# Kernel tuning notes

Hardware: AMD Instinct MI355X
Metric: run time of the kernel (lower is better)

The kernel has to match this reference:

```python
import jax, jax.numpy as jnp
import numpy as np

ALPHA = 0.2          # LeakyReLU negative slope
NEG_BIG = -9e15      # mask value from original code


def setup_inputs() -> dict:
    key = jax.random.key(0)
    k1, k2, k3, k4 = jax.random.split(key, 4)
    B, N, F_in, F_out = 16, 1024, 256, 256
    x = jax.random.normal(k1, (B, N, F_in), dtype=jnp.float32)
    adj = jax.random.randint(k2, (B, N, N), 0, 2, dtype=jnp.int32)
    # xavier-uniform-like scales
    W = jax.random.normal(k3, (F_in, F_out), dtype=jnp.float32) * np.sqrt(2.0 / (F_in + F_out))
    a = jax.random.normal(k4, (2 * F_out, 1), dtype=jnp.float32) * np.sqrt(2.0 / (2 * F_out + 1))
    return {"x": x, "adj": adj, "W": W, "a": a}


def reference(x, adj, W, a):
    # x: [B,N,Fin], adj: [B,N,N] (int mask), W: [Fin,Fout], a: [2*Fout,1]
    F_out = a.shape[0] // 2
    h = jnp.einsum("bni,io->bno", x, W)            # [B,N,Fout]
    # Decompose a into left/right halves: e_ij = lrelu(a_l.h_i + a_r.h_j)
    a_l = a[:F_out, 0]                               # [Fout]
    a_r = a[F_out:, 0]                               # [Fout]
    el = h @ a_l                                     # [B,N] score contribution of target i
    er = h @ a_r                                     # [B,N] score contribution of source j
    e = jax.nn.leaky_relu(el[:, :, None] + er[:, None, :], ALPHA)  # [B,N,N]
    e = jnp.where(adj > 0, e, NEG_BIG)
    attn = jax.nn.softmax(e, axis=-1)                # masked softmax over neighbors j
    # weighted sum of neighbor features; concat with n_heads=1 is identity
    return jnp.einsum("bij,bjo->bio", attn, h)       # [B,N,Fout]
```

## Files before the change

kernel.cpp:

```cpp
#include <hip/hip_runtime.h>
#include <stdint.h>

#define ALPHA 0.2f

typedef __attribute__((ext_vector_type(8))) short bf16x8;
typedef __attribute__((ext_vector_type(8))) unsigned short u16x8;
typedef __attribute__((ext_vector_type(4))) float f32x4;

__device__ __forceinline__ unsigned short f2bf(float f) {
    unsigned int u = __float_as_uint(f);
    u += 0x7fffu + ((u >> 16) & 1u);
    return (unsigned short)(u >> 16);
}

__device__ __forceinline__ void gload_lds16(const void* g, void* l) {
    __builtin_amdgcn_global_load_lds(
        (const __attribute__((address_space(1))) unsigned int*)g,
        (__attribute__((address_space(3))) unsigned int*)l, 16, 0, 0);
}

__global__ void wt_wa_kernel(const float* __restrict__ W,
                             const float* __restrict__ a,
                             unsigned short* __restrict__ Wtbf,
                             float* __restrict__ wa) {
    const int t = threadIdx.x;
    if (blockIdx.x < 256) {
        const int o = blockIdx.x;
        Wtbf[o * 256 + t] = f2bf(W[t * 256 + o]);
    } else {
        float sl = 0.f, sr = 0.f;
        const float* wr = W + t * 256;
        for (int o = 0; o < 256; ++o) {
            const float wv = wr[o];
            sl += wv * a[o];
            sr += wv * a[256 + o];
        }
        wa[t] = sl;
        wa[256 + t] = sr;
    }
}

__global__ __launch_bounds__(256) void gemm_hx(
    const unsigned short* __restrict__ Wtbf,
    const float* __restrict__ x,
    const float* __restrict__ wa,
    unsigned short* __restrict__ hT,
    float* __restrict__ el, float* __restrict__ er)
{
    __shared__ __align__(16) unsigned short As[64 * 256];
    __shared__ float wa_s[512];

    const int tid = threadIdx.x;
    const int w = tid >> 6, l = tid & 63;
    const int q = l >> 4, ml = l & 15;
    const int wm = (w >> 1) * 32;
    const int wn = (w & 1) * 64;
    const int m0 = blockIdx.y * 64;
    const int n0 = blockIdx.x * 128;

    if (tid < 128) *(float4*)(wa_s + tid * 4) = *(const float4*)(wa + tid * 4);

    for (int rd = 0; rd < 8; ++rd) {
        const int cb = rd * 256 + (w << 6);
        const int p = cb + l;
        const int r = p >> 5;
        const int c = p & 31;
        gload_lds16(Wtbf + (size_t)(m0 + r) * 256 + ((c ^ (r & 7)) << 3),
                    As + cb * 8);
    }
    __syncthreads();

    const bool do_e = (blockIdx.y == 0) && (w < 2);

    f32x4 acc[2][4];
    for (int i = 0; i < 2; ++i)
        for (int j = 0; j < 4; ++j) {
            f32x4 z = {0.f, 0.f, 0.f, 0.f};
            acc[i][j] = z;
        }
    float sl[4] = {0.f, 0.f, 0.f, 0.f};
    float sr[4] = {0.f, 0.f, 0.f, 0.f};

    for (int k0 = 0; k0 < 256; k0 += 64) {
        bf16x8 aF[2][2], bF[2][4];
#pragma unroll
        for (int ks = 0; ks < 2; ++ks) {
            const int kb = k0 + ks * 32 + q * 8;
#pragma unroll
            for (int mt = 0; mt < 2; ++mt) {
                const int row = wm + mt * 16 + ml;
                const int cf = (kb >> 3) ^ (row & 7);
                aF[ks][mt] = *(const bf16x8*)(As + (row * 32 + cf) * 8);
            }
#pragma unroll
            for (int nt = 0; nt < 4; ++nt) {
                const int grow = n0 + wn + nt * 16 + ml;
                const float* xp = x + (size_t)grow * 256 + kb;
                const float4 v0 = *(const float4*)(xp);
                const float4 v1 = *(const float4*)(xp + 4);
                bf16x8 f;
                f[0] = (short)f2bf(v0.x); f[1] = (short)f2bf(v0.y);
                f[2] = (short)f2bf(v0.z); f[3] = (short)f2bf(v0.w);
                f[4] = (short)f2bf(v1.x); f[5] = (short)f2bf(v1.y);
                f[6] = (short)f2bf(v1.z); f[7] = (short)f2bf(v1.w);
                bF[ks][nt] = f;
                if (do_e) {
                    const float* wl = wa_s + kb;
                    const float* wrr = wa_s + 256 + kb;
                    sl[nt] += v0.x * wl[0] + v0.y * wl[1] + v0.z * wl[2] + v0.w * wl[3]
                            + v1.x * wl[4] + v1.y * wl[5] + v1.z * wl[6] + v1.w * wl[7];
                    sr[nt] += v0.x * wrr[0] + v0.y * wrr[1] + v0.z * wrr[2] + v0.w * wrr[3]
                            + v1.x * wrr[4] + v1.y * wrr[5] + v1.z * wrr[6] + v1.w * wrr[7];
                }
            }
        }
#pragma unroll
        for (int ks = 0; ks < 2; ++ks)
            for (int mt = 0; mt < 2; ++mt)
                for (int nt = 0; nt < 4; ++nt)
                    acc[mt][nt] = __builtin_amdgcn_mfma_f32_16x16x32_bf16(
                        aF[ks][mt], bF[ks][nt], acc[mt][nt], 0, 0, 0);
    }

    if (do_e) {
#pragma unroll
        for (int nt = 0; nt < 4; ++nt) {
            sl[nt] += __shfl_xor(sl[nt], 16); sl[nt] += __shfl_xor(sl[nt], 32);
            sr[nt] += __shfl_xor(sr[nt], 16); sr[nt] += __shfl_xor(sr[nt], 32);
        }
        if (l < 16) {
#pragma unroll
            for (int nt = 0; nt < 4; ++nt) {
                const int n = n0 + wn + nt * 16 + l;
                el[n] = sl[nt];
                er[n] = sr[nt];
            }
        }
    }

    for (int mt = 0; mt < 2; ++mt)
        for (int nt = 0; nt < 4; ++nt) {
            const int gn = n0 + wn + nt * 16 + ml;
            for (int r = 0; r < 4; ++r) {
                const int gm = m0 + wm + mt * 16 + q * 4 + r;
                hT[(size_t)gm * 16384 + gn] = f2bf(acc[mt][nt][r]);
            }
        }
}

__global__ __launch_bounds__(256) void pv_fused(
    const int* __restrict__ adj,
    const float* __restrict__ el,
    const float* __restrict__ er,
    const unsigned short* __restrict__ hT,
    float* __restrict__ out)
{
    __shared__ float er_s[1024];
    __shared__ float el_s[32];
    __shared__ float c_s[32];
    __shared__ __align__(16) unsigned short pk_s[32 * 64];
    __shared__ __align__(16) unsigned char buf[8192];
    __shared__ __align__(16) unsigned short Hs[256 * 64];

    unsigned char (*nibs)[256] = (unsigned char (*)[256])buf;
    unsigned short* Ps = (unsigned short*)buf;

    const int tid = threadIdx.x;
    const int w = tid >> 6, l = tid & 63;
    const int q = l >> 4, ml = l & 15;
    const int b = blockIdx.y;
    const int i0 = blockIdx.x * 32;

    *(float4*)(er_s + tid * 4) = *(const float4*)(er + (b << 10) + tid * 4);
    if (tid < 32) el_s[tid] = el[(b << 10) + i0 + tid];
    __syncthreads();

    const float NINF = -__builtin_inff();
    const float* erb = er + (b << 10);
    for (int rr = 0; rr < 8; ++rr) {
        const int row = w * 8 + rr;
        const int* arow = adj + (size_t)((b << 10) + i0 + row) * 1024;
        const float eli = el_s[row];

        int4 av[4]; float4 erv[4];
#pragma unroll
        for (int it = 0; it < 4; ++it) {
            const int j = it * 256 + l * 4;
            av[it]  = *(const int4*)(arow + j);
            erv[it] = *(const float4*)(erb + j);
        }
        float s = 0.f;
#pragma unroll
        for (int it = 0; it < 4; ++it) {
            float e0 = eli + erv[it].x; e0 = e0 > 0.f ? e0 : ALPHA * e0;
            float e1 = eli + erv[it].y; e1 = e1 > 0.f ? e1 : ALPHA * e1;
            float e2 = eli + erv[it].z; e2 = e2 > 0.f ? e2 : ALPHA * e2;
            float e3 = eli + erv[it].w; e3 = e3 > 0.f ? e3 : ALPHA * e3;
            e0 = av[it].x > 0 ? e0 : NINF;
            e1 = av[it].y > 0 ? e1 : NINF;
            e2 = av[it].z > 0 ? e2 : NINF;
            e3 = av[it].w > 0 ? e3 : NINF;
            s += __expf(e0) + __expf(e1) + __expf(e2) + __expf(e3);
            nibs[row][it * 64 + l] =
                (unsigned char)((av[it].x > 0) | ((av[it].y > 0) << 1) |
                                ((av[it].z > 0) << 2) | ((av[it].w > 0) << 3));
        }
#pragma unroll
        for (int off = 32; off >= 1; off >>= 1) s += __shfl_xor(s, off);
        if (l == 0) c_s[row] = __logf(s);
    }
    for (int rr = 0; rr < 8; ++rr) {
        const int row = w * 8 + rr;
        const unsigned nr = *(const unsigned int*)(&nibs[row][l * 4]);
        pk_s[row * 64 + l] =
            (unsigned short)((nr & 0xFu) | ((nr >> 4) & 0xF0u) |
                             ((nr >> 8) & 0xF00u) | ((nr >> 12) & 0xF000u));
    }
    __syncthreads();

    const int ib = tid >> 3;
    const int js = (tid & 7) * 8;
    const float eli_b = el_s[ib];
    const float ci = c_s[ib];

    f32x4 acc[2][4];
    for (int i = 0; i < 2; ++i)
        for (int j = 0; j < 4; ++j) {
            f32x4 z = {0.f, 0.f, 0.f, 0.f};
            acc[i][j] = z;
        }

    const unsigned short* hb = hT + (size_t)b * 1024;

    for (int j0 = 0; j0 < 1024; j0 += 64) {
        for (int cr = 0; cr < 8; ++cr) {
            const int cb = cr * 256 + (w << 6);
            const int p = cb + l;
            const int r = p >> 3;
            const int cc = (p & 7) ^ (r & 7);
            gload_lds16(hb + (size_t)r * 16384 + j0 + cc * 8, Hs + cb * 8);
        }
        {
            const unsigned hw = pk_s[ib * 64 + ((j0 + js) >> 4)];
            const unsigned v = (hw >> ((j0 + js) & 15)) & 0xFFu;
            u16x8 pvv;
#pragma unroll
            for (int u = 0; u < 8; ++u) {
                float e = eli_b + er_s[j0 + js + u];
                e = e > 0.f ? e : ALPHA * e;
                const float p = ((v >> u) & 1u) ? __expf(e - ci) : 0.f;
                pvv[u] = f2bf(p);
            }
            *(u16x8*)(Ps + ib * 72 + js) = pvv;
        }
        __syncthreads();

        bf16x8 aF[2][2], bF[2][4];
#pragma unroll
        for (int ks = 0; ks < 2; ++ks) {
#pragma unroll
            for (int mt = 0; mt < 2; ++mt)
                aF[ks][mt] = *(const bf16x8*)(Ps + (mt * 16 + ml) * 72 + ks * 32 + q * 8);
#pragma unroll
            for (int nt = 0; nt < 4; ++nt) {
                const int oc = (w << 6) + nt * 16 + ml;
                bF[ks][nt] = *(const bf16x8*)(Hs + (oc * 8 + ((ks * 4 + q) ^ (oc & 7))) * 8);
            }
        }
#pragma unroll
        for (int ks = 0; ks < 2; ++ks)
            for (int mt = 0; mt < 2; ++mt)
                for (int nt = 0; nt < 4; ++nt)
                    acc[mt][nt] = __builtin_amdgcn_mfma_f32_16x16x32_bf16(
                        aF[ks][mt], bF[ks][nt], acc[mt][nt], 0, 0, 0);
        __syncthreads();
    }

    float* ob = out + (size_t)b * 262144;
    for (int mt = 0; mt < 2; ++mt)
        for (int nt = 0; nt < 4; ++nt) {
            const int gn = (w << 6) + nt * 16 + ml;
            for (int r = 0; r < 4; ++r) {
                const int gm = i0 + mt * 16 + q * 4 + r;
                ob[(size_t)gm * 256 + gn] = acc[mt][nt][r];
            }
        }
}

extern "C" void kernel_launch(void* const* d_in, const int* in_sizes, int n_in,
                              void* d_out, int out_size, void* d_ws, size_t ws_size,
                              hipStream_t stream) {
    const float* x   = (const float*)d_in[0];
    const int*   adj = (const int*)d_in[1];
    const float* W   = (const float*)d_in[2];
    const float* a   = (const float*)d_in[3];
    float* out = (float*)d_out;

    char* ws = (char*)d_ws;
    unsigned short* Wtbf = (unsigned short*)(ws);
    float* wa            = (float*)(ws + 131072);
    unsigned short* h_T  = (unsigned short*)(ws + 133120);
    float* el            = (float*)(ws + 8521728);
    float* er            = (float*)(ws + 8587264);

    wt_wa_kernel<<<dim3(257), dim3(256), 0, stream>>>(W, a, Wtbf, wa);

    gemm_hx<<<dim3(128, 4), dim3(256), 0, stream>>>(Wtbf, x, wa, h_T, el, er);

    pv_fused<<<dim3(32, 16), dim3(256), 0, stream>>>(adj, el, er, h_T, out);
}
```

Baseline: 163.2 us.

## Split adjacency mask/softmax-normalizer pass into a separate high-parallelism kernel

Moves the adjacency read, bit-packing and log-sum-exp normalizer computation out of the fused PV kernel into a standalone mask_kernel with one wave per row across 4096 blocks. The PV kernel then loads a small precomputed 16-bit packed mask and per-row constants instead of streaming the 64MB int adjacency itself. The aim is to spread the bandwidth-bound adjacency scan over many more blocks than the 512-block PV grid. The cost is an extra kernel launch and a workspace round trip for the packed mask and normalizers.

```diff
diff --git a/kernel.cpp b/kernel.cpp
--- a/kernel.cpp
+++ b/kernel.cpp
@@ -148,22 +148,70 @@
         }
 }
 
-__global__ __launch_bounds__(256) void pv_fused(
+__global__ __launch_bounds__(256) void mask_kernel(
     const int* __restrict__ adj,
     const float* __restrict__ el,
     const float* __restrict__ er,
+    float* __restrict__ c,
+    unsigned short* __restrict__ pk16)
+{
+    __shared__ unsigned char nibs[4][256];
+
+    const int w = threadIdx.x >> 6, l = threadIdx.x & 63;
+    const int row = blockIdx.x * 4 + w;
+    const int b = row >> 10;
+    const int* arow = adj + (size_t)row * 1024;
+    const float* erb = er + (b << 10);
+    const float eli = el[row];
+
+    int4 av[4]; float4 erv[4];
+#pragma unroll
+    for (int it = 0; it < 4; ++it) {
+        const int j = it * 256 + l * 4;
+        av[it]  = *(const int4*)(arow + j);
+        erv[it] = *(const float4*)(erb + j);
+    }
+
+    const float NINF = -__builtin_inff();
+    float s = 0.f;
+#pragma unroll
+    for (int it = 0; it < 4; ++it) {
+        float e0 = eli + erv[it].x; e0 = e0 > 0.f ? e0 : ALPHA * e0;
+        float e1 = eli + erv[it].y; e1 = e1 > 0.f ? e1 : ALPHA * e1;
+        float e2 = eli + erv[it].z; e2 = e2 > 0.f ? e2 : ALPHA * e2;
+        float e3 = eli + erv[it].w; e3 = e3 > 0.f ? e3 : ALPHA * e3;
+        e0 = av[it].x > 0 ? e0 : NINF;
+        e1 = av[it].y > 0 ? e1 : NINF;
+        e2 = av[it].z > 0 ? e2 : NINF;
+        e3 = av[it].w > 0 ? e3 : NINF;
+        s += __expf(e0) + __expf(e1) + __expf(e2) + __expf(e3);
+        nibs[w][it * 64 + l] =
+            (unsigned char)((av[it].x > 0) | ((av[it].y > 0) << 1) |
+                            ((av[it].z > 0) << 2) | ((av[it].w > 0) << 3));
+    }
+#pragma unroll
+    for (int off = 32; off >= 1; off >>= 1) s += __shfl_xor(s, off);
+    if (l == 0) c[row] = __logf(s);
+
+    const unsigned nr = *(const unsigned int*)(&nibs[w][l * 4]);
+    const unsigned short mask16 =
+        (unsigned short)((nr & 0xFu) | ((nr >> 4) & 0xF0u) |
+                         ((nr >> 8) & 0xF00u) | ((nr >> 12) & 0xF000u));
+    pk16[(size_t)row * 64 + l] = mask16;
+}
+
+__global__ __launch_bounds__(256) void pv_kernel(
+    const unsigned short* __restrict__ pk16,
+    const float* __restrict__ el,
+    const float* __restrict__ er,
+    const float* __restrict__ c,
     const unsigned short* __restrict__ hT,
     float* __restrict__ out)
 {
     __shared__ float er_s[1024];
-    __shared__ float el_s[32];
-    __shared__ float c_s[32];
     __shared__ __align__(16) unsigned short pk_s[32 * 64];
-    __shared__ __align__(16) unsigned char buf[8192];
     __shared__ __align__(16) unsigned short Hs[256 * 64];
-
-    unsigned char (*nibs)[256] = (unsigned char (*)[256])buf;
-    unsigned short* Ps = (unsigned short*)buf;
+    __shared__ __align__(16) unsigned short Ps[32 * 72];
 
     const int tid = threadIdx.x;
     const int w = tid >> 6, l = tid & 63;
@@ -172,56 +220,13 @@
     const int i0 = blockIdx.x * 32;
 
     *(float4*)(er_s + tid * 4) = *(const float4*)(er + (b << 10) + tid * 4);
-    if (tid < 32) el_s[tid] = el[(b << 10) + i0 + tid];
-    __syncthreads();
-
-    const float NINF = -__builtin_inff();
-    const float* erb = er + (b << 10);
-    for (int rr = 0; rr < 8; ++rr) {
-        const int row = w * 8 + rr;
-        const int* arow = adj + (size_t)((b << 10) + i0 + row) * 1024;
-        const float eli = el_s[row];
-
-        int4 av[4]; float4 erv[4];
-#pragma unroll
-        for (int it = 0; it < 4; ++it) {
-            const int j = it * 256 + l * 4;
-            av[it]  = *(const int4*)(arow + j);
-            erv[it] = *(const float4*)(erb + j);
-        }
-        float s = 0.f;
-#pragma unroll
-        for (int it = 0; it < 4; ++it) {
-            float e0 = eli + erv[it].x; e0 = e0 > 0.f ? e0 : ALPHA * e0;
-            float e1 = eli + erv[it].y; e1 = e1 > 0.f ? e1 : ALPHA * e1;
-            float e2 = eli + erv[it].z; e2 = e2 > 0.f ? e2 : ALPHA * e2;
-            float e3 = eli + erv[it].w; e3 = e3 > 0.f ? e3 : ALPHA * e3;
-            e0 = av[it].x > 0 ? e0 : NINF;
-            e1 = av[it].y > 0 ? e1 : NINF;
-            e2 = av[it].z > 0 ? e2 : NINF;
-            e3 = av[it].w > 0 ? e3 : NINF;
-            s += __expf(e0) + __expf(e1) + __expf(e2) + __expf(e3);
-            nibs[row][it * 64 + l] =
-                (unsigned char)((av[it].x > 0) | ((av[it].y > 0) << 1) |
-                                ((av[it].z > 0) << 2) | ((av[it].w > 0) << 3));
-        }
-#pragma unroll
-        for (int off = 32; off >= 1; off >>= 1) s += __shfl_xor(s, off);
-        if (l == 0) c_s[row] = __logf(s);
-    }
-    for (int rr = 0; rr < 8; ++rr) {
-        const int row = w * 8 + rr;
-        const unsigned nr = *(const unsigned int*)(&nibs[row][l * 4]);
-        pk_s[row * 64 + l] =
-            (unsigned short)((nr & 0xFu) | ((nr >> 4) & 0xF0u) |
-                             ((nr >> 8) & 0xF00u) | ((nr >> 12) & 0xF000u));
-    }
-    __syncthreads();
-
+    *(u16x8*)(pk_s + tid * 8) =
+        *(const u16x8*)(pk16 + ((size_t)(b << 10) + i0) * 64 + tid * 8);
     const int ib = tid >> 3;
     const int js = (tid & 7) * 8;
-    const float eli_b = el_s[ib];
-    const float ci = c_s[ib];
+    const float eli_b = el[(b << 10) + i0 + ib];
+    const float ci = c[(b << 10) + i0 + ib];
+    __syncthreads();
 
     f32x4 acc[2][4];
     for (int i = 0; i < 2; ++i)
@@ -302,10 +307,14 @@
     unsigned short* h_T  = (unsigned short*)(ws + 133120);
     float* el            = (float*)(ws + 8521728);
     float* er            = (float*)(ws + 8587264);
+    float* c             = (float*)(ws + 8652800);
+    unsigned short* pk16 = (unsigned short*)(ws + 8718336);
 
     wt_wa_kernel<<<dim3(257), dim3(256), 0, stream>>>(W, a, Wtbf, wa);
 
     gemm_hx<<<dim3(128, 4), dim3(256), 0, stream>>>(Wtbf, x, wa, h_T, el, er);
 
-    pv_fused<<<dim3(32, 16), dim3(256), 0, stream>>>(adj, el, er, h_T, out);
-}
+    mask_kernel<<<dim3(4096), dim3(256), 0, stream>>>(adj, el, er, c, pk16);
+
+    pv_kernel<<<dim3(32, 16), dim3(256), 0, stream>>>(pk16, el, er, c, h_T, out);
+}
```

New measurement: 165.1 us. Within noise of the previous version (+1.2%).
